# Optimization experiments

Hardware: AMD Instinct MI355X
Metric: run time of the kernel (lower is better)

## Reference

```python
import jax, jax.numpy as jnp
import numpy as np

D_MODEL = 1024
D_STATE = 16
D_CONV = 4
EXPAND = 2
D_INNER = EXPAND * D_MODEL          # 2048
DT_RANK = (D_MODEL + 15) // 16      # 64
B_SZ, L = 2, 2048


def setup_inputs() -> dict:
    key = jax.random.key(0)
    ks = jax.random.split(key, 14)
    s = 0.02
    dt_init = jax.random.uniform(ks[10], (D_INNER,), minval=1e-3, maxval=0.1)
    A = jnp.tile(jnp.arange(1, D_STATE + 1, dtype=jnp.float32)[None, :], (D_INNER, 1))
    return {
        "x_f": jax.random.normal(ks[0], (B_SZ, L, D_MODEL), jnp.float32),
        "x_h": jax.random.normal(ks[1], (B_SZ, L, D_MODEL), jnp.float32),
        "W_hf": s * jax.random.normal(ks[2], (D_MODEL, D_MODEL), jnp.float32),
        "b_hf": jnp.zeros((D_MODEL,), jnp.float32),
        "W_in": s * jax.random.normal(ks[3], (2 * D_INNER, D_MODEL), jnp.float32),
        "conv_w": s * jax.random.normal(ks[4], (D_INNER, 1, D_CONV), jnp.float32),
        "conv_b": jnp.zeros((D_INNER,), jnp.float32),
        "W_x": s * jax.random.normal(ks[5], (DT_RANK + 2 * D_STATE, D_INNER), jnp.float32),
        "W_dt": (DT_RANK ** -0.5) * jax.random.normal(ks[6], (D_INNER, DT_RANK), jnp.float32),
        "b_dt": jnp.log(jnp.expm1(dt_init)),
        "A_log": jnp.log(A),
        "D": jnp.ones((D_INNER,), jnp.float32),
        "W_out": s * jax.random.normal(ks[7], (D_MODEL, D_INNER), jnp.float32),
    }


def _mamba(x, W_in, conv_w, conv_b, W_x, W_dt, b_dt, A_log, D, W_out):
    B, Lx, _ = x.shape
    # in_proj -> x, z branches  [B, L, 2*d_inner]
    xz = jnp.einsum("bld,ed->ble", x, W_in)
    x_in, z = jnp.split(xz, 2, axis=-1)
    # causal depthwise conv1d, kernel d_conv, groups = d_inner
    x_nch = jnp.transpose(x_in, (0, 2, 1))  # [B, d_inner, L]
    x_conv = jax.lax.conv_general_dilated(
        x_nch, conv_w, window_strides=(1,), padding=[(D_CONV - 1, 0)],
        dimension_numbers=("NCH", "OIH", "NCH"), feature_group_count=D_INNER)
    x_c = jax.nn.silu(jnp.transpose(x_conv, (0, 2, 1)) + conv_b)  # [B, L, d_inner]
    # input-dependent dt, B, C
    x_dbl = jnp.einsum("ble,fe->blf", x_c, W_x)
    dt_r = x_dbl[..., :DT_RANK]
    B_ssm = x_dbl[..., DT_RANK:DT_RANK + D_STATE]          # [B, L, d_state]
    C_ssm = x_dbl[..., DT_RANK + D_STATE:]                  # [B, L, d_state]
    dt = jax.nn.softplus(jnp.einsum("blr,er->ble", dt_r, W_dt) + b_dt)  # [B, L, d_inner]
    A = -jnp.exp(A_log)  # [d_inner, d_state]

    # selective scan over time; carry h: [B, d_inner, d_state]
    def step(h, inp):
        dt_t, B_t, C_t, x_t = inp  # [B,d_inner], [B,d_state], [B,d_state], [B,d_inner]
        dA = jnp.exp(dt_t[:, :, None] * A)                       # [B, d_inner, d_state]
        dBx = dt_t[:, :, None] * B_t[:, None, :] * x_t[:, :, None]
        h = dA * h + dBx
        y_t = jnp.einsum("bes,bs->be", h, C_t)
        return h, y_t

    seq = (jnp.transpose(dt, (1, 0, 2)), jnp.transpose(B_ssm, (1, 0, 2)),
           jnp.transpose(C_ssm, (1, 0, 2)), jnp.transpose(x_c, (1, 0, 2)))
    h0 = jnp.zeros((B, D_INNER, D_STATE), x.dtype)
    _, ys = jax.lax.scan(step, h0, seq)
    y = jnp.transpose(ys, (1, 0, 2)) + D * x_c   # skip term
    y = y * jax.nn.silu(z)                        # output gate
    return jnp.einsum("ble,de->bld", y, W_out)


def reference(x_f, x_h, W_hf, b_hf, W_in, conv_w, conv_b, W_x, W_dt, b_dt, A_log, D, W_out):
    hf_gate = jax.nn.sigmoid(jnp.einsum("bld,ed->ble", x_h, W_hf) + b_hf)
    modulated = x_f * hf_gate
    return _mamba(modulated, W_in, conv_w, conv_b, W_x, W_dt, b_dt, A_log, D, W_out)
```

## Files before the change

### kernel.cpp

```cpp
#include <hip/hip_runtime.h>
#include <hip/hip_bf16.h>
#include <math.h>

#define L_SEQ  2048
#define BATCH  2
#define DMODEL 1024
#define DINNER 2048
#define DSTATE 16
#define NCHUNK 32
#define LCH    (L_SEQ / NCHUNK)

typedef __attribute__((ext_vector_type(8))) short bf16x8;
typedef __attribute__((ext_vector_type(4))) float f32x4;

__device__ __forceinline__ unsigned short f2bu(float x) {
    __hip_bfloat16 h = __float2bfloat16(x);
    return __builtin_bit_cast(unsigned short, h);
}
__device__ __forceinline__ float fast_exp2(float x) {
    float r; asm("v_exp_f32 %0, %1" : "=v"(r) : "v"(x)); return r;
}
#define LOG2E 1.44269504088896f

__global__ __launch_bounds__(256) void cvt_all(
    const float* __restrict__ Wout, const float* __restrict__ Win,
    const float* __restrict__ xh,   const float* __restrict__ Whf,
    const float* __restrict__ Wx,   const float* __restrict__ Wdt,
    __hip_bfloat16* __restrict__ dWout, __hip_bfloat16* __restrict__ dWin,
    __hip_bfloat16* __restrict__ dxh,   __hip_bfloat16* __restrict__ dWhf,
    __hip_bfloat16* __restrict__ dWx,   __hip_bfloat16* __restrict__ dWdt)
{
    int bid = blockIdx.x;
    const float* s; __hip_bfloat16* d;
    if (bid < 2048)       { s = Wout; d = dWout; }
    else if (bid < 6144)  { s = Win;  d = dWin;  bid -= 2048; }
    else if (bid < 10240) { s = xh;   d = dxh;   bid -= 6144; }
    else if (bid < 11264) { s = Whf;  d = dWhf;  bid -= 10240; }
    else if (bid < 11520) {
        bid -= 11264;
        const int i = (bid * 256 + threadIdx.x) * 4;
        const int r = i >> 11;
        ushort4 u = {0, 0, 0, 0};
        if (r < 96) {
            const float4 v = *reinterpret_cast<const float4*>(&Wx[i]);
            u.x = f2bu(v.x); u.y = f2bu(v.y); u.z = f2bu(v.z); u.w = f2bu(v.w);
        }
        *reinterpret_cast<ushort4*>(&dWx[i]) = u;
        return;
    }
    else                  { s = Wdt;  d = dWdt;  bid -= 11520; }
    const int i = (bid * 256 + threadIdx.x) * 4;
    const float4 v = *reinterpret_cast<const float4*>(&s[i]);
    ushort4 u;
    u.x = f2bu(v.x); u.y = f2bu(v.y); u.z = f2bu(v.z); u.w = f2bu(v.w);
    *reinterpret_cast<ushort4*>(&d[i]) = u;
}

template <int EPI>
__global__ __launch_bounds__(256) void mfma_gemm(
    const __hip_bfloat16* __restrict__ A, int lda,
    const __hip_bfloat16* __restrict__ Bw, int ldb,
    int ksz,
    float* __restrict__ Cf, int ldc,
    __hip_bfloat16* __restrict__ Cb,
    __hip_bfloat16* __restrict__ Cb2,
    const float* __restrict__ bias,
    const float* __restrict__ mul, int ldmul)
{
    __shared__ unsigned short As[3][128 * 32];
    __shared__ unsigned short Bs[3][128 * 32];
    const int tid = threadIdx.x;
    const int row0 = blockIdx.y * 128;
    const int col0 = blockIdx.x * 128;
    const int wid = tid >> 6, lane = tid & 63;
    const int wr = wid >> 1, wc = wid & 1;
    const int fr = lane & 15, fq = lane >> 4;
    const int kz0 = blockIdx.z * ksz;

    f32x4 acc[4][4];
#pragma unroll
    for (int i = 0; i < 4; i++)
#pragma unroll
        for (int j = 0; j < 4; j++) acc[i][j] = (f32x4){0.f, 0.f, 0.f, 0.f};

    const int i0 = tid, i1 = tid + 256;
    const size_t ga0 = (size_t)(row0 + (i0 >> 2)) * lda + (i0 & 3) * 8;
    const size_t ga1 = (size_t)(row0 + (i1 >> 2)) * lda + (i1 & 3) * 8;
    const size_t gb0 = (size_t)(col0 + (i0 >> 2)) * ldb + (i0 & 3) * 8;
    const size_t gb1 = (size_t)(col0 + (i1 >> 2)) * ldb + (i1 & 3) * 8;
    const int nk = ksz >> 5;

#if __has_builtin(__builtin_amdgcn_global_load_lds)
    auto STAGE = [&](int buf, int koff) {
        __builtin_amdgcn_global_load_lds(
            (const __attribute__((address_space(1))) unsigned int*)(A + ga0 + koff),
            (__attribute__((address_space(3))) unsigned int*)&As[buf][i0 * 8], 16, 0, 0);
        __builtin_amdgcn_global_load_lds(
            (const __attribute__((address_space(1))) unsigned int*)(A + ga1 + koff),
            (__attribute__((address_space(3))) unsigned int*)&As[buf][i1 * 8], 16, 0, 0);
        __builtin_amdgcn_global_load_lds(
            (const __attribute__((address_space(1))) unsigned int*)(Bw + gb0 + koff),
            (__attribute__((address_space(3))) unsigned int*)&Bs[buf][i0 * 8], 16, 0, 0);
        __builtin_amdgcn_global_load_lds(
            (const __attribute__((address_space(1))) unsigned int*)(Bw + gb1 + koff),
            (__attribute__((address_space(3))) unsigned int*)&Bs[buf][i1 * 8], 16, 0, 0);
    };
    STAGE(0, kz0);
    STAGE(1, kz0 + 32);
    asm volatile("s_waitcnt vmcnt(4)" ::: "memory");
    __builtin_amdgcn_s_barrier();
    __builtin_amdgcn_sched_barrier(0);
    for (int kk = 0; kk < nk; kk++) {
        const int cur = kk % 3;
        if (kk + 2 < nk) STAGE((kk + 2) % 3, kz0 + (kk + 2) * 32);
        bf16x8 af[4], bq[4];
#pragma unroll
        for (int rb = 0; rb < 4; rb++)
            af[rb] = *reinterpret_cast<const bf16x8*>(
                &As[cur][(wr * 64 + rb * 16 + fr) * 32 + fq * 8]);
#pragma unroll
        for (int cb = 0; cb < 4; cb++)
            bq[cb] = *reinterpret_cast<const bf16x8*>(
                &Bs[cur][(wc * 64 + cb * 16 + fr) * 32 + fq * 8]);
#pragma unroll
        for (int rb = 0; rb < 4; rb++)
#pragma unroll
            for (int cb = 0; cb < 4; cb++)
                acc[rb][cb] = __builtin_amdgcn_mfma_f32_16x16x32_bf16(
                    af[rb], bq[cb], acc[rb][cb], 0, 0, 0);
        if (kk + 1 < nk) {
            if (kk + 2 < nk) {
                asm volatile("s_waitcnt vmcnt(4)" ::: "memory");
            } else {
                asm volatile("s_waitcnt vmcnt(0)" ::: "memory");
            }
            __builtin_amdgcn_s_barrier();
            __builtin_amdgcn_sched_barrier(0);
        }
    }
#else
    for (int kk = 0; kk < nk; kk++) {
        const int koff = kz0 + kk * 32;
        const uint4 va0 = *reinterpret_cast<const uint4*>(A + ga0 + koff);
        const uint4 va1 = *reinterpret_cast<const uint4*>(A + ga1 + koff);
        const uint4 vb0 = *reinterpret_cast<const uint4*>(Bw + gb0 + koff);
        const uint4 vb1 = *reinterpret_cast<const uint4*>(Bw + gb1 + koff);
        __syncthreads();
        *reinterpret_cast<uint4*>(&As[0][i0 * 8]) = va0;
        *reinterpret_cast<uint4*>(&As[0][i1 * 8]) = va1;
        *reinterpret_cast<uint4*>(&Bs[0][i0 * 8]) = vb0;
        *reinterpret_cast<uint4*>(&Bs[0][i1 * 8]) = vb1;
        __syncthreads();
        bf16x8 af[4], bq[4];
#pragma unroll
        for (int rb = 0; rb < 4; rb++)
            af[rb] = *reinterpret_cast<const bf16x8*>(
                &As[0][(wr * 64 + rb * 16 + fr) * 32 + fq * 8]);
#pragma unroll
        for (int cb = 0; cb < 4; cb++)
            bq[cb] = *reinterpret_cast<const bf16x8*>(
                &Bs[0][(wc * 64 + cb * 16 + fr) * 32 + fq * 8]);
#pragma unroll
        for (int rb = 0; rb < 4; rb++)
#pragma unroll
            for (int cb = 0; cb < 4; cb++)
                acc[rb][cb] = __builtin_amdgcn_mfma_f32_16x16x32_bf16(
                    af[rb], bq[cb], acc[rb][cb], 0, 0, 0);
    }
#endif

    float* Cz = Cf;
    if (EPI == 0)
        Cz = Cf + (size_t)blockIdx.z * (size_t)(gridDim.y * 128) * ldc;
    const int r0 = row0 + wr * 64, c0 = col0 + wc * 64;
#pragma unroll
    for (int rb = 0; rb < 4; rb++)
#pragma unroll
        for (int cb = 0; cb < 4; cb++) {
            const int col = c0 + cb * 16 + fr;
#pragma unroll
            for (int j = 0; j < 4; j++) {
                const int row = r0 + rb * 16 + fq * 4 + j;
                float v = acc[rb][cb][j];
                if (EPI == 0) {
                    Cz[(size_t)row * ldc + col] = v;
                } else if (EPI == 1) {
                    v = 1.f / (1.f + __expf(-(v + bias[col])));
                    v *= mul[(size_t)row * ldmul + col];
                    Cb[(size_t)row * ldc + col] = __float2bfloat16(v);
                } else if (EPI == 2) {
                    if (col0 < 2048) Cb[(size_t)row * 2048 + col] = __float2bfloat16(v);
                    else             Cb2[(size_t)row * 2048 + col - 2048] = __float2bfloat16(v);
                } else {
                    v += bias[col];
                    v = (v > 20.f) ? v : log1pf(__expf(v));
                    Cf[(size_t)row * ldc + col] = v;
                }
            }
        }
}

__global__ __launch_bounds__(256) void reduce_xdbl(
    const float* __restrict__ part, float* __restrict__ xdbl,
    __hip_bfloat16* __restrict__ dtr)
{
    const int i = blockIdx.x * 256 + threadIdx.x;
    float s = 0.f;
#pragma unroll
    for (int j = 0; j < 8; j++) s += part[(size_t)j * 524288 + i];
    xdbl[i] = s;
    const int col = i & 127;
    if (col < 64) dtr[((i >> 7) << 6) + col] = __float2bfloat16(s);
}

__global__ __launch_bounds__(256) void conv_silu_kernel(
    const __hip_bfloat16* __restrict__ xin_b, const float* __restrict__ cw,
    const float* __restrict__ cb, __hip_bfloat16* __restrict__ xcb)
{
    int gid = blockIdx.x * 256 + threadIdx.x;
    int e = gid & (DINNER - 1);
    int row = gid >> 11;
    int t = row & (L_SEQ - 1);
    float s = cb[e];
#pragma unroll
    for (int j = 0; j < 4; j++) {
        int tt = t - 3 + j;
        if (tt >= 0)
            s = fmaf(cw[e * 4 + j],
                     __bfloat162float(xin_b[(size_t)(row - 3 + j) * 2048 + e]), s);
    }
    xcb[(size_t)row * 2048 + e] = __float2bfloat16(s / (1.f + __expf(-s)));
}

__global__ __launch_bounds__(256) void scan_pass_a(
    const float* __restrict__ dtp, const __hip_bfloat16* __restrict__ xcb,
    const float* __restrict__ xdbl, const float* __restrict__ A_log,
    float* __restrict__ hloc, float* __restrict__ Pp)
{
    __shared__ float sB[LCH][16];
    const int tid = threadIdx.x;
    const int e = (blockIdx.x << 8) + tid;
    const int chunk = blockIdx.y;
    const int b = blockIdx.z;
    const int t0 = chunk * LCH;

    {
        const int r = tid >> 2, sl = tid & 3;
        *(float4*)&sB[r][sl * 4] =
            *(const float4*)&xdbl[(size_t)(b * L_SEQ + t0 + r) * 128 + 64 + sl * 4];
    }
    float av[16];
#pragma unroll
    for (int sq = 0; sq < 4; sq++) {
        const float4 al = *(const float4*)&A_log[e * 16 + sq * 4];
#pragma unroll
        for (int j = 0; j < 4; j++)
            av[sq * 4 + j] = -fast_exp2(((const float*)&al)[j] * LOG2E);
    }
    float h[16];
#pragma unroll
    for (int s = 0; s < 16; s++) h[s] = 0.f;
    float sdt = 0.f;
    __syncthreads();

    const size_t rb = (size_t)(b * L_SEQ + t0) * 2048 + e;
    float dtv_n = dtp[rb];
    float xv_n = __bfloat162float(xcb[rb]);
    for (int t = 0; t < LCH; t++) {
        const float dtv = dtv_n, xv = xv_n;
        if (t + 1 < LCH) {
            dtv_n = dtp[rb + (size_t)(t + 1) * 2048];
            xv_n = __bfloat162float(xcb[rb + (size_t)(t + 1) * 2048]);
        }
        sdt += dtv;
        const float dtx = dtv * xv;
        const float dl2 = dtv * LOG2E;
#pragma unroll
        for (int sq = 0; sq < 4; sq++) {
            const float4 B4 = *(const float4*)&sB[t][sq * 4];
#pragma unroll
            for (int j = 0; j < 4; j++) {
                const int s = sq * 4 + j;
                const float Bv = ((const float*)&B4)[j];
                h[s] = fmaf(fast_exp2(dl2 * av[s]), h[s], Bv * dtx);
            }
        }
    }
    const size_t o = (((size_t)chunk * BATCH + b) * 2048 + e) * 16;
#pragma unroll
    for (int sq = 0; sq < 4; sq++) {
        *(float4*)&hloc[o + sq * 4] =
            make_float4(h[sq * 4], h[sq * 4 + 1], h[sq * 4 + 2], h[sq * 4 + 3]);
        *(float4*)&Pp[o + sq * 4] = make_float4(
            fast_exp2(av[sq * 4] * sdt * LOG2E),
            fast_exp2(av[sq * 4 + 1] * sdt * LOG2E),
            fast_exp2(av[sq * 4 + 2] * sdt * LOG2E),
            fast_exp2(av[sq * 4 + 3] * sdt * LOG2E));
    }
}

__global__ __launch_bounds__(256) void scan_pass_b(
    const float* __restrict__ hloc, const float* __restrict__ Pp,
    float* __restrict__ h0)
{
    const int idx = blockIdx.x * 256 + threadIdx.x;
    float h = 0.f;
    h0[idx] = 0.f;
    for (int c = 0; c < NCHUNK - 1; c++) {
        h = fmaf(Pp[(size_t)c * 65536 + idx], h, hloc[(size_t)c * 65536 + idx]);
        h0[(size_t)(c + 1) * 65536 + idx] = h;
    }
}

__global__ __launch_bounds__(256) void scan_pass_c(
    const float* __restrict__ dtp, const __hip_bfloat16* __restrict__ xcb,
    const float* __restrict__ xdbl, const __hip_bfloat16* __restrict__ zb,
    const float* __restrict__ A_log, const float* __restrict__ Dw,
    const float* __restrict__ h0, __hip_bfloat16* __restrict__ yb)
{
    __shared__ float sB[LCH][16];
    __shared__ float sC[LCH][16];
    const int tid = threadIdx.x;
    const int e = (blockIdx.x << 8) + tid;
    const int chunk = blockIdx.y;
    const int b = blockIdx.z;
    const int t0 = chunk * LCH;

    {
        const int r = tid >> 2, sl = tid & 3;
        const size_t base = (size_t)(b * L_SEQ + t0 + r) * 128;
        *(float4*)&sB[r][sl * 4] = *(const float4*)&xdbl[base + 64 + sl * 4];
        *(float4*)&sC[r][sl * 4] = *(const float4*)&xdbl[base + 80 + sl * 4];
    }
    float av[16];
#pragma unroll
    for (int sq = 0; sq < 4; sq++) {
        const float4 al = *(const float4*)&A_log[e * 16 + sq * 4];
#pragma unroll
        for (int j = 0; j < 4; j++)
            av[sq * 4 + j] = -fast_exp2(((const float*)&al)[j] * LOG2E);
    }
    const float De = Dw[e];
    float h[16];
    const size_t o = (((size_t)chunk * BATCH + b) * 2048 + e) * 16;
#pragma unroll
    for (int sq = 0; sq < 4; sq++) {
        const float4 hv = *(const float4*)&h0[o + sq * 4];
        h[sq * 4] = hv.x; h[sq * 4 + 1] = hv.y;
        h[sq * 4 + 2] = hv.z; h[sq * 4 + 3] = hv.w;
    }
    __syncthreads();

    const size_t rb = (size_t)(b * L_SEQ + t0) * 2048 + e;
    float dtv_n = dtp[rb];
    float xv_n = __bfloat162float(xcb[rb]);
    float zv_n = __bfloat162float(zb[rb]);
    for (int t = 0; t < LCH; t++) {
        const float dtv = dtv_n, xv = xv_n, zv = zv_n;
        if (t + 1 < LCH) {
            dtv_n = dtp[rb + (size_t)(t + 1) * 2048];
            xv_n = __bfloat162float(xcb[rb + (size_t)(t + 1) * 2048]);
            zv_n = __bfloat162float(zb[rb + (size_t)(t + 1) * 2048]);
        }
        const float dtx = dtv * xv;
        const float dl2 = dtv * LOG2E;
        float yp0 = 0.f, yp1 = 0.f, yp2 = 0.f, yp3 = 0.f;
#pragma unroll
        for (int sq = 0; sq < 4; sq++) {
            const float4 B4 = *(const float4*)&sB[t][sq * 4];
            const float4 C4 = *(const float4*)&sC[t][sq * 4];
#pragma unroll
            for (int j = 0; j < 4; j++) {
                const int s = sq * 4 + j;
                const float Bv = ((const float*)&B4)[j];
                const float Cv = ((const float*)&C4)[j];
                h[s] = fmaf(fast_exp2(dl2 * av[s]), h[s], Bv * dtx);
                if (sq == 0) yp0 = fmaf(h[s], Cv, yp0);
                else if (sq == 1) yp1 = fmaf(h[s], Cv, yp1);
                else if (sq == 2) yp2 = fmaf(h[s], Cv, yp2);
                else yp3 = fmaf(h[s], Cv, yp3);
            }
        }
        float yv = (yp0 + yp1) + (yp2 + yp3);
        yv = fmaf(De, xv, yv);
        const float sig = 1.f / (1.f + __expf(-zv));
        yb[rb + (size_t)t * 2048] = __float2bfloat16(yv * zv * sig);
    }
}

extern "C" void kernel_launch(void* const* d_in, const int* in_sizes, int n_in,
                              void* d_out, int out_size, void* d_ws, size_t ws_size,
                              hipStream_t stream)
{
    const float* x_f    = (const float*)d_in[0];
    const float* x_h    = (const float*)d_in[1];
    const float* W_hf   = (const float*)d_in[2];
    const float* b_hf   = (const float*)d_in[3];
    const float* W_in   = (const float*)d_in[4];
    const float* conv_w = (const float*)d_in[5];
    const float* conv_b = (const float*)d_in[6];
    const float* W_x    = (const float*)d_in[7];
    const float* W_dt   = (const float*)d_in[8];
    const float* b_dt   = (const float*)d_in[9];
    const float* A_log  = (const float*)d_in[10];
    const float* Dw     = (const float*)d_in[11];
    const float* W_out  = (const float*)d_in[12];
    float* out = (float*)d_out;
    float* ws  = (float*)d_ws;

    __hip_bfloat16* wout_b = (__hip_bfloat16*)(ws);
    __hip_bfloat16* win_b  = (__hip_bfloat16*)(ws + 1048576);
    __hip_bfloat16* xh_b   = (__hip_bfloat16*)(ws + 3145728);
    __hip_bfloat16* whf_b  = (__hip_bfloat16*)(ws + 5242880);
    __hip_bfloat16* m_b    = (__hip_bfloat16*)(ws + 5767168);
    float*          hloc   = ws + 1048576;
    float*          Pp     = ws + 3145728;
    float*          h0     = ws + 5242880;
    __hip_bfloat16* wx_b   = (__hip_bfloat16*)(ws + 7864320);
    __hip_bfloat16* wdt_b  = (__hip_bfloat16*)(ws + 7995392);
    __hip_bfloat16* dtr_b  = (__hip_bfloat16*)(ws + 8060928);
    float*          xdbl   = ws + 10289152;
    __hip_bfloat16* xin_b  = (__hip_bfloat16*)(ws + 10813440);
    __hip_bfloat16* z_b    = (__hip_bfloat16*)(ws + 15007744);
    __hip_bfloat16* xc_b   = (__hip_bfloat16*)(ws + 19202048);
    float*          part   = ws + 23396352;
    float*          dtp    = ws + 23396352;
    __hip_bfloat16* yb     = (__hip_bfloat16*)(ws + 31784960);

    cvt_all<<<11648, 256, 0, stream>>>(
        W_out, W_in, x_h, W_hf, W_x, W_dt,
        wout_b, win_b, xh_b, whf_b, wx_b, wdt_b);

    mfma_gemm<1><<<dim3(8, 32, 1), 256, 0, stream>>>(
        xh_b, DMODEL, whf_b, DMODEL, DMODEL,
        nullptr, DMODEL, m_b, nullptr, b_hf, x_f, DMODEL);

    mfma_gemm<2><<<dim3(32, 32, 1), 256, 0, stream>>>(
        m_b, DMODEL, win_b, DMODEL, DMODEL,
        nullptr, 2048, xin_b, z_b, nullptr, nullptr, 0);

    conv_silu_kernel<<<32768, 256, 0, stream>>>(
        xin_b, conv_w, conv_b, xc_b);

    mfma_gemm<0><<<dim3(1, 32, 8), 256, 0, stream>>>(
        xc_b, DINNER, wx_b, DINNER, 256,
        part, 128, nullptr, nullptr, nullptr, nullptr, 0);
    reduce_xdbl<<<2048, 256, 0, stream>>>(part, xdbl, dtr_b);

    mfma_gemm<3><<<dim3(16, 32, 1), 256, 0, stream>>>(
        dtr_b, 64, wdt_b, 64, 64,
        dtp, 2048, nullptr, nullptr, b_dt, nullptr, 0);

    scan_pass_a<<<dim3(8, NCHUNK - 1, BATCH), 256, 0, stream>>>(
        dtp, xc_b, xdbl, A_log, hloc, Pp);
    scan_pass_b<<<256, 256, 0, stream>>>(hloc, Pp, h0);
    scan_pass_c<<<dim3(8, NCHUNK, BATCH), 256, 0, stream>>>(
        dtp, xc_b, xdbl, z_b, A_log, Dw, h0, yb);

    mfma_gemm<0><<<dim3(8, 32, 1), 256, 0, stream>>>(
        yb, DINNER, wout_b, DINNER, DINNER,
        out, DMODEL, nullptr, nullptr, nullptr, nullptr, 0);
}
```

Before: 313.7 us.

## Shrink GEMM tile to 64x128, drop triple buffering, store dt as bf16

The GEMM kernel moves from 128x128 tiles with a three-stage global_load_lds pipeline to 64x128 tiles with a single LDS buffer and two syncthreads per k-step, doubling the grid in y. The dt projection epilogue now writes bf16 instead of fp32, and both scan passes read the bf16 dt. This raises block count and occupancy and halves dt memory traffic, but gives up load/compute overlap and lowers per-block data reuse. It also loses some dt precision.

```diff
diff --git a/kernel.cpp b/kernel.cpp
--- a/kernel.cpp
+++ b/kernel.cpp
@@ -67,114 +67,74 @@
     const float* __restrict__ bias,
     const float* __restrict__ mul, int ldmul)
 {
-    __shared__ unsigned short As[3][128 * 32];
-    __shared__ unsigned short Bs[3][128 * 32];
+    __shared__ unsigned short As[64 * 32];
+    __shared__ unsigned short Bs[128 * 32];
     const int tid = threadIdx.x;
-    const int row0 = blockIdx.y * 128;
+    const int row0 = blockIdx.y * 64;
     const int col0 = blockIdx.x * 128;
     const int wid = tid >> 6, lane = tid & 63;
     const int wr = wid >> 1, wc = wid & 1;
     const int fr = lane & 15, fq = lane >> 4;
     const int kz0 = blockIdx.z * ksz;
 
-    f32x4 acc[4][4];
-#pragma unroll
-    for (int i = 0; i < 4; i++)
+    f32x4 acc[2][4];
+#pragma unroll
+    for (int i = 0; i < 2; i++)
 #pragma unroll
         for (int j = 0; j < 4; j++) acc[i][j] = (f32x4){0.f, 0.f, 0.f, 0.f};
 
-    const int i0 = tid, i1 = tid + 256;
-    const size_t ga0 = (size_t)(row0 + (i0 >> 2)) * lda + (i0 & 3) * 8;
-    const size_t ga1 = (size_t)(row0 + (i1 >> 2)) * lda + (i1 & 3) * 8;
-    const size_t gb0 = (size_t)(col0 + (i0 >> 2)) * ldb + (i0 & 3) * 8;
-    const size_t gb1 = (size_t)(col0 + (i1 >> 2)) * ldb + (i1 & 3) * 8;
+    const size_t ga  = (size_t)(row0 + (tid >> 2)) * lda + (tid & 3) * 8;
+    const size_t gb0 = (size_t)(col0 + (tid >> 2)) * ldb + (tid & 3) * 8;
+    const size_t gb1 = (size_t)(col0 + 64 + (tid >> 2)) * ldb + (tid & 3) * 8;
     const int nk = ksz >> 5;
 
+    for (int kk = 0; kk < nk; kk++) {
+        const int koff = kz0 + kk * 32;
 #if __has_builtin(__builtin_amdgcn_global_load_lds)
-    auto STAGE = [&](int buf, int koff) {
+        __syncthreads();
         __builtin_amdgcn_global_load_lds(
-            (const __attribute__((address_space(1))) unsigned int*)(A + ga0 + koff),
-            (__attribute__((address_space(3))) unsigned int*)&As[buf][i0 * 8], 16, 0, 0);
-        __builtin_amdgcn_global_load_lds(
-            (const __attribute__((address_space(1))) unsigned int*)(A + ga1 + koff),
-            (__attribute__((address_space(3))) unsigned int*)&As[buf][i1 * 8], 16, 0, 0);
+            (const __attribute__((address_space(1))) unsigned int*)(A + ga + koff),
+            (__attribute__((address_space(3))) unsigned int*)&As[tid * 8], 16, 0, 0);
         __builtin_amdgcn_global_load_lds(
             (const __attribute__((address_space(1))) unsigned int*)(Bw + gb0 + koff),
-            (__attribute__((address_space(3))) unsigned int*)&Bs[buf][i0 * 8], 16, 0, 0);
+            (__attribute__((address_space(3))) unsigned int*)&Bs[tid * 8], 16, 0, 0);
         __builtin_amdgcn_global_load_lds(
             (const __attribute__((address_space(1))) unsigned int*)(Bw + gb1 + koff),
-            (__attribute__((address_space(3))) unsigned int*)&Bs[buf][i1 * 8], 16, 0, 0);
-    };
-    STAGE(0, kz0);
-    STAGE(1, kz0 + 32);
-    asm volatile("s_waitcnt vmcnt(4)" ::: "memory");
-    __builtin_amdgcn_s_barrier();
-    __builtin_amdgcn_sched_barrier(0);
-    for (int kk = 0; kk < nk; kk++) {
-        const int cur = kk % 3;
-        if (kk + 2 < nk) STAGE((kk + 2) % 3, kz0 + (kk + 2) * 32);
-        bf16x8 af[4], bq[4];
-#pragma unroll
-        for (int rb = 0; rb < 4; rb++)
+            (__attribute__((address_space(3))) unsigned int*)&Bs[2048 + tid * 8], 16, 0, 0);
+        __syncthreads();
+#else
+        const uint4 va  = *reinterpret_cast<const uint4*>(A + ga + koff);
+        const uint4 vb0 = *reinterpret_cast<const uint4*>(Bw + gb0 + koff);
+        const uint4 vb1 = *reinterpret_cast<const uint4*>(Bw + gb1 + koff);
+        __syncthreads();
+        *reinterpret_cast<uint4*>(&As[tid * 8]) = va;
+        *reinterpret_cast<uint4*>(&Bs[tid * 8]) = vb0;
+        *reinterpret_cast<uint4*>(&Bs[2048 + tid * 8]) = vb1;
+        __syncthreads();
+#endif
+        bf16x8 af[2], bq[4];
+#pragma unroll
+        for (int rb = 0; rb < 2; rb++)
             af[rb] = *reinterpret_cast<const bf16x8*>(
-                &As[cur][(wr * 64 + rb * 16 + fr) * 32 + fq * 8]);
+                &As[(wr * 32 + rb * 16 + fr) * 32 + fq * 8]);
 #pragma unroll
         for (int cb = 0; cb < 4; cb++)
             bq[cb] = *reinterpret_cast<const bf16x8*>(
-                &Bs[cur][(wc * 64 + cb * 16 + fr) * 32 + fq * 8]);
-#pragma unroll
-        for (int rb = 0; rb < 4; rb++)
+                &Bs[(wc * 64 + cb * 16 + fr) * 32 + fq * 8]);
+#pragma unroll
+        for (int rb = 0; rb < 2; rb++)
 #pragma unroll
             for (int cb = 0; cb < 4; cb++)
                 acc[rb][cb] = __builtin_amdgcn_mfma_f32_16x16x32_bf16(
                     af[rb], bq[cb], acc[rb][cb], 0, 0, 0);
-        if (kk + 1 < nk) {
-            if (kk + 2 < nk) {
-                asm volatile("s_waitcnt vmcnt(4)" ::: "memory");
-            } else {
-                asm volatile("s_waitcnt vmcnt(0)" ::: "memory");
-            }
-            __builtin_amdgcn_s_barrier();
-            __builtin_amdgcn_sched_barrier(0);
-        }
-    }
-#else
-    for (int kk = 0; kk < nk; kk++) {
-        const int koff = kz0 + kk * 32;
-        const uint4 va0 = *reinterpret_cast<const uint4*>(A + ga0 + koff);
-        const uint4 va1 = *reinterpret_cast<const uint4*>(A + ga1 + koff);
-        const uint4 vb0 = *reinterpret_cast<const uint4*>(Bw + gb0 + koff);
-        const uint4 vb1 = *reinterpret_cast<const uint4*>(Bw + gb1 + koff);
-        __syncthreads();
-        *reinterpret_cast<uint4*>(&As[0][i0 * 8]) = va0;
-        *reinterpret_cast<uint4*>(&As[0][i1 * 8]) = va1;
-        *reinterpret_cast<uint4*>(&Bs[0][i0 * 8]) = vb0;
-        *reinterpret_cast<uint4*>(&Bs[0][i1 * 8]) = vb1;
-        __syncthreads();
-        bf16x8 af[4], bq[4];
-#pragma unroll
-        for (int rb = 0; rb < 4; rb++)
-            af[rb] = *reinterpret_cast<const bf16x8*>(
-                &As[0][(wr * 64 + rb * 16 + fr) * 32 + fq * 8]);
-#pragma unroll
-        for (int cb = 0; cb < 4; cb++)
-            bq[cb] = *reinterpret_cast<const bf16x8*>(
-                &Bs[0][(wc * 64 + cb * 16 + fr) * 32 + fq * 8]);
-#pragma unroll
-        for (int rb = 0; rb < 4; rb++)
-#pragma unroll
-            for (int cb = 0; cb < 4; cb++)
-                acc[rb][cb] = __builtin_amdgcn_mfma_f32_16x16x32_bf16(
-                    af[rb], bq[cb], acc[rb][cb], 0, 0, 0);
-    }
-#endif
+    }
 
     float* Cz = Cf;
     if (EPI == 0)
-        Cz = Cf + (size_t)blockIdx.z * (size_t)(gridDim.y * 128) * ldc;
-    const int r0 = row0 + wr * 64, c0 = col0 + wc * 64;
-#pragma unroll
-    for (int rb = 0; rb < 4; rb++)
+        Cz = Cf + (size_t)blockIdx.z * (size_t)(gridDim.y * 64) * ldc;
+    const int r0 = row0 + wr * 32, c0 = col0 + wc * 64;
+#pragma unroll
+    for (int rb = 0; rb < 2; rb++)
 #pragma unroll
         for (int cb = 0; cb < 4; cb++) {
             const int col = c0 + cb * 16 + fr;
@@ -194,7 +154,7 @@
                 } else {
                     v += bias[col];
                     v = (v > 20.f) ? v : log1pf(__expf(v));
-                    Cf[(size_t)row * ldc + col] = v;
+                    Cb[(size_t)row * ldc + col] = __float2bfloat16(v);
                 }
             }
         }
@@ -233,7 +193,7 @@
 }
 
 __global__ __launch_bounds__(256) void scan_pass_a(
-    const float* __restrict__ dtp, const __hip_bfloat16* __restrict__ xcb,
+    const __hip_bfloat16* __restrict__ dtb, const __hip_bfloat16* __restrict__ xcb,
     const float* __restrict__ xdbl, const float* __restrict__ A_log,
     float* __restrict__ hloc, float* __restrict__ Pp)
 {
@@ -264,12 +224,12 @@
     __syncthreads();
 
     const size_t rb = (size_t)(b * L_SEQ + t0) * 2048 + e;
-    float dtv_n = dtp[rb];
+    float dtv_n = __bfloat162float(dtb[rb]);
     float xv_n = __bfloat162float(xcb[rb]);
     for (int t = 0; t < LCH; t++) {
         const float dtv = dtv_n, xv = xv_n;
         if (t + 1 < LCH) {
-            dtv_n = dtp[rb + (size_t)(t + 1) * 2048];
+            dtv_n = __bfloat162float(dtb[rb + (size_t)(t + 1) * 2048]);
             xv_n = __bfloat162float(xcb[rb + (size_t)(t + 1) * 2048]);
         }
         sdt += dtv;
@@ -313,7 +273,7 @@
 }
 
 __global__ __launch_bounds__(256) void scan_pass_c(
-    const float* __restrict__ dtp, const __hip_bfloat16* __restrict__ xcb,
+    const __hip_bfloat16* __restrict__ dtb, const __hip_bfloat16* __restrict__ xcb,
     const float* __restrict__ xdbl, const __hip_bfloat16* __restrict__ zb,
     const float* __restrict__ A_log, const float* __restrict__ Dw,
     const float* __restrict__ h0, __hip_bfloat16* __restrict__ yb)
@@ -352,13 +312,13 @@
     __syncthreads();
 
     const size_t rb = (size_t)(b * L_SEQ + t0) * 2048 + e;
-    float dtv_n = dtp[rb];
+    float dtv_n = __bfloat162float(dtb[rb]);
     float xv_n = __bfloat162float(xcb[rb]);
     float zv_n = __bfloat162float(zb[rb]);
     for (int t = 0; t < LCH; t++) {
         const float dtv = dtv_n, xv = xv_n, zv = zv_n;
         if (t + 1 < LCH) {
-            dtv_n = dtp[rb + (size_t)(t + 1) * 2048];
+            dtv_n = __bfloat162float(dtb[rb + (size_t)(t + 1) * 2048]);
             xv_n = __bfloat162float(xcb[rb + (size_t)(t + 1) * 2048]);
             zv_n = __bfloat162float(zb[rb + (size_t)(t + 1) * 2048]);
         }
@@ -424,40 +384,40 @@
     __hip_bfloat16* z_b    = (__hip_bfloat16*)(ws + 15007744);
     __hip_bfloat16* xc_b   = (__hip_bfloat16*)(ws + 19202048);
     float*          part   = ws + 23396352;
-    float*          dtp    = ws + 23396352;
+    __hip_bfloat16* dt_b   = (__hip_bfloat16*)(ws + 27590656);
     __hip_bfloat16* yb     = (__hip_bfloat16*)(ws + 31784960);
 
     cvt_all<<<11648, 256, 0, stream>>>(
         W_out, W_in, x_h, W_hf, W_x, W_dt,
         wout_b, win_b, xh_b, whf_b, wx_b, wdt_b);
 
-    mfma_gemm<1><<<dim3(8, 32, 1), 256, 0, stream>>>(
+    mfma_gemm<1><<<dim3(8, 64, 1), 256, 0, stream>>>(
         xh_b, DMODEL, whf_b, DMODEL, DMODEL,
         nullptr, DMODEL, m_b, nullptr, b_hf, x_f, DMODEL);
 
-    mfma_gemm<2><<<dim3(32, 32, 1), 256, 0, stream>>>(
+    mfma_gemm<2><<<dim3(32, 64, 1), 256, 0, stream>>>(
         m_b, DMODEL, win_b, DMODEL, DMODEL,
         nullptr, 2048, xin_b, z_b, nullptr, nullptr, 0);
 
     conv_silu_kernel<<<32768, 256, 0, stream>>>(
         xin_b, conv_w, conv_b, xc_b);
 
-    mfma_gemm<0><<<dim3(1, 32, 8), 256, 0, stream>>>(
+    mfma_gemm<0><<<dim3(1, 64, 8), 256, 0, stream>>>(
         xc_b, DINNER, wx_b, DINNER, 256,
         part, 128, nullptr, nullptr, nullptr, nullptr, 0);
     reduce_xdbl<<<2048, 256, 0, stream>>>(part, xdbl, dtr_b);
 
-    mfma_gemm<3><<<dim3(16, 32, 1), 256, 0, stream>>>(
+    mfma_gemm<3><<<dim3(16, 64, 1), 256, 0, stream>>>(
         dtr_b, 64, wdt_b, 64, 64,
-        dtp, 2048, nullptr, nullptr, b_dt, nullptr, 0);
+        nullptr, 2048, dt_b, nullptr, b_dt, nullptr, 0);
 
     scan_pass_a<<<dim3(8, NCHUNK - 1, BATCH), 256, 0, stream>>>(
-        dtp, xc_b, xdbl, A_log, hloc, Pp);
+        dt_b, xc_b, xdbl, A_log, hloc, Pp);
     scan_pass_b<<<256, 256, 0, stream>>>(hloc, Pp, h0);
     scan_pass_c<<<dim3(8, NCHUNK, BATCH), 256, 0, stream>>>(
-        dtp, xc_b, xdbl, z_b, A_log, Dw, h0, yb);
-
-    mfma_gemm<0><<<dim3(8, 32, 1), 256, 0, stream>>>(
+        dt_b, xc_b, xdbl, z_b, A_log, Dw, h0, yb);
+
+    mfma_gemm<0><<<dim3(8, 64, 1), 256, 0, stream>>>(
         yb, DINNER, wout_b, DINNER, DINNER,
         out, DMODEL, nullptr, nullptr, nullptr, nullptr, 0);
 }
```

Result: faster. 304.2 us (-3.0%).
